# Performance work log

Measured on AMD Instinct MI355X. Metric: run time of the kernel, lower is better.

## Reference

```python
import jax, jax.numpy as jnp
import numpy as np

M = 1024      # num_inducing
B = 131072    # batch of query points (original module is per-query; we vmap/vectorize)
EPS_D = 1e-8
JITTER = 1e-4

Z_SCALE = np.array([0.15, 0.1, 0.05, 800.0, 20.0], dtype=np.float32)
Z_SHIFT = np.array([0.0, 0.0, 0.0, 600.0, 5.0], dtype=np.float32)


def setup_inputs() -> dict:
    key = jax.random.key(0)
    k1, k2 = jax.random.split(key)
    x_star = jax.random.normal(k1, (B, 5), dtype=jnp.float32)
    # learnable params, sized/initialized per the flax module
    log_lengthscale = jnp.log(jnp.array([0.2, 0.15, 0.1, 400.0, 15.0], dtype=jnp.float32))
    log_variance = jnp.asarray(jnp.log(0.08), dtype=jnp.float32)
    Z_raw = jax.random.uniform(k2, (M, 5), dtype=jnp.float32)  # uniform(scale=1.0) init
    return {"x_star": x_star, "log_lengthscale": log_lengthscale,
            "log_variance": log_variance, "Z_raw": Z_raw}


def _pairwise_sqdist(A, Bm):
    # ||a-b||^2 via gemm; A:(n,d), Bm:(m,d) -> (n,m)
    aa = jnp.sum(A * A, axis=-1)
    bb = jnp.sum(Bm * Bm, axis=-1)
    d2 = aa[:, None] + bb[None, :] - 2.0 * (A @ Bm.T)
    return jnp.maximum(d2, 0.0)


def _matern52(d2, prior_var):
    d = jnp.sqrt(d2 + EPS_D)
    s = jnp.sqrt(5.0) * d
    return prior_var * (1.0 + s + (5.0 / 3.0) * (d * d)) * jnp.exp(-s)


def reference(x_star, log_lengthscale, log_variance, Z_raw):
    ls = jnp.exp(log_lengthscale)                # (5,)
    prior_var = jnp.exp(log_variance)            # scalar
    Z = Z_raw * jnp.asarray(Z_SCALE) + jnp.asarray(Z_SHIFT)  # (M,5)
    inv_ls = 1.0 / (ls + 1e-8)
    Zs = Z * inv_ls                              # lengthscale-scaled inducing pts
    Xs = x_star * inv_ls                         # (B,5)

    K_ZZ = _matern52(_pairwise_sqdist(Zs, Zs), prior_var)            # (M,M)
    K_ZZ_inv = jnp.linalg.inv(K_ZZ + JITTER * jnp.eye(M, dtype=K_ZZ.dtype))

    k_xZ = _matern52(_pairwise_sqdist(Xs, Zs), prior_var)            # (B,M)
    red = jnp.sum(k_xZ * (k_xZ @ K_ZZ_inv), axis=-1)                 # (B,)
    variance = jnp.maximum(prior_var - red, 1e-6)
    return jnp.sqrt(variance)                                        # (B,) predictive std
```

## Files before the change

kernel.cpp:

```cpp
#include <hip/hip_runtime.h>
#include <math.h>

#define B_TOT 131072
#define M_N   1024
#define BS    128
#define NBK   8

typedef float    f32x4 __attribute__((ext_vector_type(4)));
typedef _Float16 f16x8 __attribute__((ext_vector_type(8)));

enum : size_t {
    OFF_KF  = 0,
    OFF_LF  = (size_t)4 << 20,
    OFF_WF  = (size_t)8 << 20,
    OFF_WPH = (size_t)12 << 20,
    OFF_WPL = (size_t)14 << 20,
    OFF_PF  = (size_t)16 << 20,
    OFF_ZT  = ((size_t)16 << 20) + 256,
};

__device__ __constant__ float c_zscale[5] = {0.15f, 0.1f, 0.05f, 800.0f, 20.0f};
__device__ __constant__ float c_zshift[5] = {0.0f, 0.0f, 0.0f, 600.0f, 5.0f};

__global__ __launch_bounds__(256) void k_build(const float* __restrict__ log_ls,
                                               const float* __restrict__ log_var,
                                               const float* __restrict__ Zraw,
                                               float* __restrict__ Kf,
                                               float* __restrict__ pf,
                                               float* __restrict__ Zst) {
    __shared__ float ps[6];
    __shared__ float zsi[5];
    int tid = threadIdx.x;
    if (tid < 5) ps[tid] = 1.0f / (__expf(log_ls[tid]) + 1e-8f);
    if (tid == 5) ps[5] = __expf(log_var[0]);
    __syncthreads();
    int i = blockIdx.x >> 2;
    int j = (blockIdx.x & 3) * 256 + tid;
    if (tid < 5) zsi[tid] = (Zraw[i * 5 + tid] * c_zscale[tid] + c_zshift[tid]) * ps[tid];
    __syncthreads();
    float d2 = 0.0f;
#pragma unroll
    for (int d = 0; d < 5; ++d) {
        float zj = (Zraw[j * 5 + d] * c_zscale[d] + c_zshift[d]) * ps[d];
        float df = zsi[d] - zj;
        d2 += df * df;
    }
    float dd = d2 + 1e-8f;
    float dist = sqrtf(dd);
    float s = 2.23606798f * dist;
    float v = ps[5] * (1.0f + s + 1.66666667f * dd) * __expf(-s);
    if (i == j) v += 1e-4f;
    Kf[(size_t)i * M_N + j] = v;
    if (blockIdx.x < 4) {
        int m = blockIdx.x * 256 + tid;
#pragma unroll
        for (int d = 0; d < 5; ++d)
            Zst[d * M_N + m] = (Zraw[m * 5 + d] * c_zscale[d] + c_zshift[d]) * ps[d];
    }
    if (blockIdx.x == 4 && tid < 6) pf[tid] = ps[tid];
}

__global__ __launch_bounds__(512) void kw_diag(float* __restrict__ Kf,
                                               float* __restrict__ Wf, int kb) {
    if (blockIdx.x) return;
    __shared__ float As[128][129];
    __shared__ float sinv[128];
    int tid = threadIdx.x;
    int r0 = kb * BS;
    for (int idx = tid; idx < BS * BS; idx += 512) {
        int rr = idx >> 7, cc = idx & 127;
        As[rr][cc] = Kf[(size_t)(r0 + rr) * M_N + r0 + cc];
    }
    __syncthreads();

    int r = tid & 127, q = tid >> 7;
    for (int p = 0; p < 16; ++p) {
        int j0 = p * 8;
        for (int j = j0; j < j0 + 8; ++j) {
            if (tid == j) {
                float d = sqrtf(As[j][j]);
                As[j][j] = d;
                sinv[j] = 1.0f / d;
            }
            __syncthreads();
            float arj = 0.0f;
            if (q == 0 && r > j) {
                arj = As[r][j] * sinv[j];
                As[r][j] = arj;
            }
            __syncthreads();
            if (q == 0 && r > j) {
#pragma unroll
                for (int c = j + 1; c < j0 + 8; ++c)
                    As[r][c] -= arj * As[c][j];
            }
        }
        __syncthreads();
        if (p < 15) {
            float a[8];
#pragma unroll
            for (int t = 0; t < 8; ++t) a[t] = As[r][j0 + t];
            for (int c = j0 + 8 + q; c < 128; c += 4) {
                if (r >= c) {
                    float s = As[r][c];
#pragma unroll
                    for (int t = 0; t < 8; ++t) s -= a[t] * As[c][j0 + t];
                    As[r][c] = s;
                }
            }
        }
        __syncthreads();
    }

    if (tid < 128) {
        int c = tid;
        for (int rb = 0; rb < 16; ++rb) {
            int r0b = rb * 8;
            if (c >= r0b + 8) continue;
            float s[8];
#pragma unroll
            for (int i = 0; i < 8; ++i) s[i] = 0.0f;
            for (int t = 0; t < r0b; ++t) {
                if (t >= c) {
                    float xt = (t == c) ? sinv[c] : As[c][t];
#pragma unroll
                    for (int i = 0; i < 8; ++i) s[i] += As[r0b + i][t] * xt;
                }
            }
            float xloc[8];
#pragma unroll
            for (int i = 0; i < 8; ++i) {
                int rr = r0b + i;
                float v = 0.0f;
                if (rr >= c) {
                    v = ((rr == c) ? 1.0f : 0.0f) - s[i];
#pragma unroll
                    for (int t2 = 0; t2 < i; ++t2) {
                        int tt = r0b + t2;
                        if (tt >= c) v -= As[rr][tt] * xloc[t2];
                    }
                    v *= sinv[rr];
                    if (rr > c) As[c][rr] = v;
                }
                xloc[i] = v;
            }
        }
    }
    __syncthreads();
    for (int idx = tid; idx < BS * BS; idx += 512) {
        int rr = idx >> 7, cc = idx & 127;
        if (rr >= cc)
            Wf[(size_t)(r0 + rr) * M_N + r0 + cc] = (rr == cc) ? sinv[rr] : As[cc][rr];
    }
}

static __device__ void d_strip(const float* __restrict__ Kf, const float* __restrict__ Wf,
                               int cb, int row0, float (*S)[129],
                               float (*Ast)[17], float (*Wst)[128], int tid) {
    int c = tid & 127, q = tid >> 7;
    float acc[32];
#pragma unroll
    for (int i = 0; i < 32; ++i) acc[i] = 0.0f;
    for (int tc = 0; tc < 8; ++tc) {
        int tb = tc * 16;
        __syncthreads();
        for (int idx = tid; idx < 64 * 16; idx += 256) {
            int rr = idx >> 4, tt = idx & 15;
            Ast[rr][tt] = Kf[(size_t)(row0 + rr) * M_N + cb + tb + tt];
        }
        for (int idx = tid; idx < 128 * 16; idx += 256) {
            int cc = idx >> 4, tt = idx & 15;
            Wst[tt][cc] = (tb + tt <= cc) ? Wf[(size_t)(cb + cc) * M_N + cb + tb + tt] : 0.0f;
        }
        __syncthreads();
#pragma unroll
        for (int t = 0; t < 16; ++t) {
            float w = Wst[t][c];
#pragma unroll
            for (int i = 0; i < 32; ++i) acc[i] += Ast[q * 32 + i][t] * w;
        }
    }
    __syncthreads();
#pragma unroll
    for (int i = 0; i < 32; ++i) S[q * 32 + i][c] = acc[i];
}

static __device__ void d_diag256(float (*As)[129], float* sinv,
                                 float* __restrict__ Wf, int r0, int tid) {
    int r = tid & 127, half = tid >> 7;
    for (int p = 0; p < 16; ++p) {
        int j0 = p * 8;
        for (int j = j0; j < j0 + 8; ++j) {
            if (tid == j) {
                float d = sqrtf(As[j][j]);
                As[j][j] = d;
                sinv[j] = 1.0f / d;
            }
            __syncthreads();
            float arj = 0.0f;
            if (half == 0 && r > j) {
                arj = As[r][j] * sinv[j];
                As[r][j] = arj;
            }
            __syncthreads();
            if (half == 0 && r > j) {
#pragma unroll
                for (int c = j + 1; c < j0 + 8; ++c)
                    As[r][c] -= arj * As[c][j];
            }
        }
        __syncthreads();
        if (p < 15) {
            float a[8];
#pragma unroll
            for (int t = 0; t < 8; ++t) a[t] = As[r][j0 + t];
            for (int c = j0 + 8 + half; c < 128; c += 2) {
                if (r >= c) {
                    float s = As[r][c];
#pragma unroll
                    for (int t = 0; t < 8; ++t) s -= a[t] * As[c][j0 + t];
                    As[r][c] = s;
                }
            }
        }
        __syncthreads();
    }
    if (tid < 128) {
        int c = tid;
        for (int rb = 0; rb < 16; ++rb) {
            int r0b = rb * 8;
            if (c >= r0b + 8) continue;
            float s[8];
#pragma unroll
            for (int i = 0; i < 8; ++i) s[i] = 0.0f;
            for (int t = 0; t < r0b; ++t) {
                if (t >= c) {
                    float xt = (t == c) ? sinv[c] : As[c][t];
#pragma unroll
                    for (int i = 0; i < 8; ++i) s[i] += As[r0b + i][t] * xt;
                }
            }
            float xloc[8];
#pragma unroll
            for (int i = 0; i < 8; ++i) {
                int rr = r0b + i;
                float v = 0.0f;
                if (rr >= c) {
                    v = ((rr == c) ? 1.0f : 0.0f) - s[i];
#pragma unroll
                    for (int t2 = 0; t2 < i; ++t2) {
                        int tt = r0b + t2;
                        if (tt >= c) v -= As[rr][tt] * xloc[t2];
                    }
                    v *= sinv[rr];
                    if (rr > c) As[c][rr] = v;
                }
                xloc[i] = v;
            }
        }
    }
    __syncthreads();
    for (int idx = tid; idx < BS * BS; idx += 256) {
        int rr = idx >> 7, cc = idx & 127;
        if (rr >= cc)
            Wf[(size_t)(r0 + rr) * M_N + r0 + cc] = (rr == cc) ? sinv[rr] : As[cc][rr];
    }
}

__global__ __launch_bounds__(256) void kw_step(float* __restrict__ Kf,
                                               float* __restrict__ Wf,
                                               float* __restrict__ Lf, int kb) {
    __shared__ float SA[64][129];
    __shared__ float SB[64][129];
    __shared__ float Ast[64][17];
    __shared__ float Wst[16][128];
    __shared__ float As[128][129];
    __shared__ float sinv[128];
    int tid = threadIdx.x;
    int base = (kb + 1) * BS;
    int cb = kb * BS;
    int tx = tid & 15, ty = tid >> 4;
    int nt = (NBK - 1 - kb) * 2;
    int ntile = nt * (nt + 1) / 2;

    if (blockIdx.x == 0) {
        d_strip(Kf, Wf, cb, base, SA, Ast, Wst, tid);
        d_strip(Kf, Wf, cb, base + 64, SB, Ast, Wst, tid);
        __syncthreads();
#pragma unroll
        for (int qq = 0; qq < 3; ++qq) {
            int qy = (qq == 0) ? 0 : 1;
            int qx = (qq == 2) ? 1 : 0;
            float (*Sy)[129] = qy ? SB : SA;
            float (*Sx)[129] = qx ? SB : SA;
            float acc[4][4];
#pragma unroll
            for (int i = 0; i < 4; ++i)
#pragma unroll
                for (int j = 0; j < 4; ++j) acc[i][j] = 0.0f;
            for (int t = 0; t < 128; ++t) {
                float a[4], b[4];
#pragma unroll
                for (int i = 0; i < 4; ++i) a[i] = Sy[ty * 4 + i][t];
#pragma unroll
                for (int j = 0; j < 4; ++j) b[j] = Sx[tx * 4 + j][t];
#pragma unroll
                for (int i = 0; i < 4; ++i)
#pragma unroll
                    for (int j = 0; j < 4; ++j) acc[i][j] = fmaf(a[i], b[j], acc[i][j]);
            }
#pragma unroll
            for (int i = 0; i < 4; ++i)
#pragma unroll
                for (int j = 0; j < 4; ++j)
                    As[qy * 64 + ty * 4 + i][qx * 64 + tx * 4 + j] =
                        Kf[(size_t)(base + qy * 64 + ty * 4 + i) * M_N +
                           base + qx * 64 + tx * 4 + j] - acc[i][j];
        }
        for (int idx = tid; idx < 64 * 128; idx += 256) {
            int rr = idx >> 7, cc = idx & 127;
            Lf[(size_t)(base + rr) * M_N + cb + cc]      = SA[rr][cc];
            Lf[(size_t)(base + 64 + rr) * M_N + cb + cc] = SB[rr][cc];
        }
        __syncthreads();
        d_diag256(As, sinv, Wf, base, tid);
    } else {
        int vp = blockIdx.x + 2;
        if (vp >= ntile) return;
        int by = 0;
        while ((by + 1) * (by + 2) / 2 <= vp) ++by;
        int bx = vp - by * (by + 1) / 2;
        int gr0 = base + by * 64, gc0 = base + bx * 64;
        d_strip(Kf, Wf, cb, gr0, SA, Ast, Wst, tid);
        if (bx != by) d_strip(Kf, Wf, cb, gc0, SB, Ast, Wst, tid);
        float (*PB)[129] = (bx == by) ? SA : SB;
        __syncthreads();
        float acc[4][4];
#pragma unroll
        for (int i = 0; i < 4; ++i)
#pragma unroll
            for (int j = 0; j < 4; ++j) acc[i][j] = 0.0f;
        for (int t = 0; t < 128; ++t) {
            float a[4], b[4];
#pragma unroll
            for (int i = 0; i < 4; ++i) a[i] = SA[ty * 4 + i][t];
#pragma unroll
            for (int j = 0; j < 4; ++j) b[j] = PB[tx * 4 + j][t];
#pragma unroll
            for (int i = 0; i < 4; ++i)
#pragma unroll
                for (int j = 0; j < 4; ++j) acc[i][j] = fmaf(a[i], b[j], acc[i][j]);
        }
#pragma unroll
        for (int i = 0; i < 4; ++i)
#pragma unroll
            for (int j = 0; j < 4; ++j)
                Kf[(size_t)(gr0 + ty * 4 + i) * M_N + gc0 + tx * 4 + j] -= acc[i][j];
        if (by == bx) {
            for (int idx = tid; idx < 64 * 128; idx += 256)
                Lf[(size_t)(gr0 + (idx >> 7)) * M_N + cb + (idx & 127)] =
                    SA[idx >> 7][idx & 127];
        }
    }
}

__global__ __launch_bounds__(512) void kw_trtri(const float* __restrict__ Lf,
                                                float* __restrict__ Wf) {
    __shared__ float Ls[128][33];
    __shared__ float Ws[32][33];
    __shared__ float Whist[6][128][33];
    __shared__ float Ps[128][33];
    int j  = blockIdx.y;
    int ct = blockIdx.x;
    int c0 = j * BS + ct * 32;
    int tid = threadIdx.x;
    int rq = tid >> 2, cq = tid & 3;

    for (int i = j + 1; i < 8; ++i) {
        float acc[8];
#pragma unroll
        for (int c = 0; c < 8; ++c) acc[c] = 0.0f;
        for (int t = j; t < i; ++t) {
            for (int ch = 0; ch < 4; ++ch) {
                int tb = t * BS + ch * 32;
                __syncthreads();
                for (int idx = tid; idx < 128 * 32; idx += 512) {
                    int rr = idx >> 5, tt = idx & 31;
                    Ls[rr][tt] = Lf[(size_t)(i * BS + rr) * M_N + tb + tt];
                }
                if (t == j) {
                    for (int idx = tid; idx < 32 * 32; idx += 512) {
                        int tt = idx >> 5, cc = idx & 31;
                        int gr = tb + tt, gc = c0 + cc;
                        Ws[tt][cc] = (gr >= gc) ? Wf[(size_t)gr * M_N + gc] : 0.0f;
                    }
                }
                __syncthreads();
                if (t == j) {
#pragma unroll
                    for (int tt = 0; tt < 32; ++tt) {
                        float l = Ls[rq][tt];
#pragma unroll
                        for (int c = 0; c < 8; ++c)
                            acc[c] = fmaf(l, Ws[tt][cq * 8 + c], acc[c]);
                    }
                } else {
                    const float (*Wh)[33] = Whist[t - j - 1];
#pragma unroll
                    for (int tt = 0; tt < 32; ++tt) {
                        float l = Ls[rq][tt];
#pragma unroll
                        for (int c = 0; c < 8; ++c)
                            acc[c] = fmaf(l, Wh[ch * 32 + tt][cq * 8 + c], acc[c]);
                    }
                }
            }
        }
        __syncthreads();
#pragma unroll
        for (int c = 0; c < 8; ++c) Ps[rq][cq * 8 + c] = acc[c];
        float a2[8];
#pragma unroll
        for (int c = 0; c < 8; ++c) a2[c] = 0.0f;
        for (int ch = 0; ch < 4; ++ch) {
            __syncthreads();
            for (int idx = tid; idx < 128 * 32; idx += 512) {
                int rr = idx >> 5, tt = idx & 31;
                Ls[rr][tt] = (rr >= ch * 32 + tt)
                           ? Wf[(size_t)(i * BS + rr) * M_N + i * BS + ch * 32 + tt] : 0.0f;
            }
            __syncthreads();
#pragma unroll
            for (int tt = 0; tt < 32; ++tt) {
                float l = Ls[rq][tt];
#pragma unroll
                for (int c = 0; c < 8; ++c)
                    a2[c] = fmaf(l, Ps[ch * 32 + tt][cq * 8 + c], a2[c]);
            }
        }
        __syncthreads();
#pragma unroll
        for (int c = 0; c < 8; ++c) {
            float v = -a2[c];
            Wf[(size_t)(i * BS + rq) * M_N + c0 + cq * 8 + c] = v;
            if (i < 7) Whist[i - j - 1][rq][cq * 8 + c] = v;
        }
        __syncthreads();
    }
}

__global__ void kw_pack(const float* __restrict__ Wf, _Float16* __restrict__ Wph,
                        _Float16* __restrict__ Wpl) {
    int T = blockIdx.x * 256 + threadIdx.x;
    int lane = T & 63, fid = T >> 6;
    int jn = fid & 63, kik = fid >> 6;
    int ki = kik & 3, kc = kik >> 2;
    int j  = jn * 16 + (lane & 15);
    int kb = kc * 128 + ki * 32 + (lane >> 4) * 8;
    f16x8 h, lo;
#pragma unroll
    for (int e = 0; e < 8; ++e) {
        int k = kb + e;
        float v = (k <= j) ? Wf[(size_t)j * M_N + k] : 0.0f;
        _Float16 hh = (_Float16)v;
        h[e]  = hh;
        lo[e] = (_Float16)(v - (float)hh);
    }
    size_t off = (size_t)fid * 512 + lane * 8;
    *(f16x8*)(Wph + off) = h;
    *(f16x8*)(Wpl + off) = lo;
}

__global__ __launch_bounds__(512, 2) void k_mm(const float* __restrict__ x_star,
                                               const float* __restrict__ pf,
                                               const float* __restrict__ Zst,
                                               const _Float16* __restrict__ Wph,
                                               const _Float16* __restrict__ Wpl,
                                               float* __restrict__ out, int Bq) {
    __shared__ __align__(16) char kls[64 * 256];
    __shared__ float red_l[64];
    int tid  = threadIdx.x;
    int slab = blockIdx.x;
    int w = tid >> 6, lane = tid & 63;
    int lrow = lane & 15, kgrp = lane >> 4;

    int scc = tid & 15, srow0 = tid >> 4;
    int q0 = slab * 64 + srow0;
    int q1 = q0 + 32;
    int qa = (q0 < Bq) ? q0 : (Bq - 1);
    int qb = (q1 < Bq) ? q1 : (Bq - 1);
    float xa0 = x_star[(size_t)qa * 5 + 0] * pf[0];
    float xa1 = x_star[(size_t)qa * 5 + 1] * pf[1];
    float xa2 = x_star[(size_t)qa * 5 + 2] * pf[2];
    float xa3 = x_star[(size_t)qa * 5 + 3] * pf[3];
    float xa4 = x_star[(size_t)qa * 5 + 4] * pf[4];
    float xb0 = x_star[(size_t)qb * 5 + 0] * pf[0];
    float xb1 = x_star[(size_t)qb * 5 + 1] * pf[1];
    float xb2 = x_star[(size_t)qb * 5 + 2] * pf[2];
    float xb3 = x_star[(size_t)qb * 5 + 3] * pf[3];
    float xb4 = x_star[(size_t)qb * 5 + 4] * pf[4];
    float pv = pf[5];
    if (tid < 64) red_l[tid] = 0.0f;

    int swz = (scc * 16) ^ ((srow0 & 15) << 4);
    int soff0 = srow0 * 256 + swz;
    int soff1 = (srow0 + 32) * 256 + swz;

    for (int pp = 0; pp < 2; ++pp) {
        f32x4 acc[4][4];
#pragma unroll
        for (int mi = 0; mi < 4; ++mi)
#pragma unroll
            for (int nj = 0; nj < 4; ++nj) acc[mi][nj] = (f32x4)(0.0f);

        int jmax_w = (pp * 32 + 24 + ((w + 3) & 7)) * 16 + 15;
        int KC = pp ? 8 : 4;

        for (int kc = 0; kc < KC; ++kc) {
            f16x8 h0, h1;
#pragma unroll
            for (int bb = 0; bb < 2; ++bb) {
                int lb = kc * 128 + scc * 8 + bb * 4;
                float z0[4], z1[4], z2[4], z3[4], z4[4];
                *(float4*)z0 = *(const float4*)&Zst[lb];
                *(float4*)z1 = *(const float4*)&Zst[M_N + lb];
                *(float4*)z2 = *(const float4*)&Zst[2 * M_N + lb];
                *(float4*)z3 = *(const float4*)&Zst[3 * M_N + lb];
                *(float4*)z4 = *(const float4*)&Zst[4 * M_N + lb];
#pragma unroll
                for (int e = 0; e < 4; ++e) {
                    float dx0 = xa0 - z0[e], dx1 = xa1 - z1[e], dx2 = xa2 - z2[e],
                          dx3 = xa3 - z3[e], dx4 = xa4 - z4[e];
                    float d2 = dx0 * dx0 + dx1 * dx1 + dx2 * dx2 + dx3 * dx3 + dx4 * dx4;
                    float dd = d2 + 1e-8f;
                    float dist = sqrtf(dd);
                    float sv = 2.23606798f * dist;
                    h0[bb * 4 + e] = (_Float16)(pv * (1.0f + sv + 1.66666667f * dd) * __expf(-sv));
                    float ex0 = xb0 - z0[e], ex1 = xb1 - z1[e], ex2 = xb2 - z2[e],
                          ex3 = xb3 - z3[e], ex4 = xb4 - z4[e];
                    float e2 = ex0 * ex0 + ex1 * ex1 + ex2 * ex2 + ex3 * ex3 + ex4 * ex4;
                    float ee = e2 + 1e-8f;
                    float edist = sqrtf(ee);
                    float esv = 2.23606798f * edist;
                    h1[bb * 4 + e] = (_Float16)(pv * (1.0f + esv + 1.66666667f * ee) * __expf(-esv));
                }
            }
            __syncthreads();
            *(f16x8*)(&kls[soff0]) = h0;
            *(f16x8*)(&kls[soff1]) = h1;
            __syncthreads();

            for (int ki = 0; ki < 4; ++ki) {
                int kmin = kc * 128 + ki * 32;
                if (kmin > jmax_w) break;
                f16x8 A_[4];
#pragma unroll
                for (int mi = 0; mi < 4; ++mi) {
                    int row = mi * 16 + lrow;
                    int cb  = ki * 64 + kgrp * 16;
                    A_[mi] = *(const f16x8*)(&kls[row * 256 + (cb ^ ((row & 15) << 4))]);
                }
#pragma unroll
                for (int nj = 0; nj < 4; ++nj) {
                    int jng = pp * 32 + nj * 8 + ((w + nj) & 7);
                    if (kmin > jng * 16 + 15) continue;
                    size_t fo = ((size_t)((kc * 4 + ki) * 64 + jng)) * 512 + lane * 8;
                    f16x8 Bh = *(const f16x8*)(Wph + fo);
                    f16x8 Bl = *(const f16x8*)(Wpl + fo);
#pragma unroll
                    for (int mi = 0; mi < 4; ++mi) {
                        acc[mi][nj] = __builtin_amdgcn_mfma_f32_16x16x32_f16(A_[mi], Bh, acc[mi][nj], 0, 0, 0);
                        acc[mi][nj] = __builtin_amdgcn_mfma_f32_16x16x32_f16(A_[mi], Bl, acc[mi][nj], 0, 0, 0);
                    }
                }
            }
        }

#pragma unroll
        for (int mi = 0; mi < 4; ++mi) {
#pragma unroll
            for (int q = 0; q < 4; ++q) {
                float s = 0.0f;
#pragma unroll
                for (int nj = 0; nj < 4; ++nj) s = fmaf(acc[mi][nj][q], acc[mi][nj][q], s);
                s += __shfl_xor(s, 1);
                s += __shfl_xor(s, 2);
                s += __shfl_xor(s, 4);
                s += __shfl_xor(s, 8);
                if (lrow == 0) atomicAdd(&red_l[mi * 16 + kgrp * 4 + q], s);
            }
        }
        __syncthreads();
    }

    if (tid < 64) {
        int b = slab * 64 + tid;
        if (b < Bq) out[b] = sqrtf(fmaxf(pv - red_l[tid], 1e-6f));
    }
}

extern "C" void kernel_launch(void* const* d_in, const int* in_sizes, int n_in,
                              void* d_out, int out_size, void* d_ws, size_t ws_size,
                              hipStream_t stream) {
    const float* x_star  = (const float*)d_in[0];
    const float* log_ls  = (const float*)d_in[1];
    const float* log_var = (const float*)d_in[2];
    const float* Z_raw   = (const float*)d_in[3];
    float* out = (float*)d_out;
    int Bq = in_sizes[0] / 5;

    char* ws = (char*)d_ws;
    float*     Kf  = (float*)(ws + OFF_KF);
    float*     Lf  = (float*)(ws + OFF_LF);
    float*     Wf  = (float*)(ws + OFF_WF);
    _Float16*  Wph = (_Float16*)(ws + OFF_WPH);
    _Float16*  Wpl = (_Float16*)(ws + OFF_WPL);
    float*     pf  = (float*)(ws + OFF_PF);
    float*     Zst = (float*)(ws + OFF_ZT);

    k_build<<<4096, 256, 0, stream>>>(log_ls, log_var, Z_raw, Kf, pf, Zst);
    kw_diag<<<64, 512, 0, stream>>>(Kf, Wf, 0);
    for (int kb = 0; kb < NBK - 1; ++kb) {
        int nt = (NBK - 1 - kb) * 2;
        int grid = nt * (nt + 1) / 2 - 2;
        if (grid < 64) grid = 64;
        kw_step<<<grid, 256, 0, stream>>>(Kf, Wf, Lf, kb);
    }
    kw_trtri<<<dim3(4, 7), 512, 0, stream>>>(Lf, Wf);
    kw_pack<<<512, 256, 0, stream>>>(Wf, Wph, Wpl);

    int slabs = (Bq + 63) / 64;
    k_mm<<<slabs, 512, 0, stream>>>(x_star, pf, Zst, Wph, Wpl, out, Bq);
}
```

Baseline: 3.510 ms.

## Compute full k_xZ row slab into LDS once, then sweep four column groups

The Matern kernel tile for all 1024 inducing points of a 64-query slab is now built once into a 128 KB LDS buffer. Previously each of two column passes rebuilt its K-chunks, so the first 512 columns' kernel values were computed twice. The matmul then loops over four column groups of two n-tiles each, cutting accumulators from 16 to 8 vectors, and drops the per-chunk double barriers. The cost is LDS use: 128 KB per block limits occupancy to one block per CU, which is why the launch-bounds minimum of 2 was removed. The exp/sqrt compute also no longer overlaps with MFMA work.

```diff
diff --git a/kernel.cpp b/kernel.cpp
--- a/kernel.cpp
+++ b/kernel.cpp
@@ -471,13 +471,13 @@
     *(f16x8*)(Wpl + off) = lo;
 }
 
-__global__ __launch_bounds__(512, 2) void k_mm(const float* __restrict__ x_star,
-                                               const float* __restrict__ pf,
-                                               const float* __restrict__ Zst,
-                                               const _Float16* __restrict__ Wph,
-                                               const _Float16* __restrict__ Wpl,
-                                               float* __restrict__ out, int Bq) {
-    __shared__ __align__(16) char kls[64 * 256];
+__global__ __launch_bounds__(512) void k_mm(const float* __restrict__ x_star,
+                                            const float* __restrict__ pf,
+                                            const float* __restrict__ Zst,
+                                            const _Float16* __restrict__ Wph,
+                                            const _Float16* __restrict__ Wpl,
+                                            float* __restrict__ out, int Bq) {
+    __shared__ __align__(16) char kls[64 * 2048];
     __shared__ float red_l[64];
     int tid  = threadIdx.x;
     int slab = blockIdx.x;
@@ -502,76 +502,73 @@
     float pv = pf[5];
     if (tid < 64) red_l[tid] = 0.0f;
 
-    int swz = (scc * 16) ^ ((srow0 & 15) << 4);
-    int soff0 = srow0 * 256 + swz;
-    int soff1 = (srow0 + 32) * 256 + swz;
-
-    for (int pp = 0; pp < 2; ++pp) {
-        f32x4 acc[4][4];
+    int swz = (srow0 & 15) << 4;
+    for (int kc = 0; kc < 8; ++kc) {
+        f16x8 h0, h1;
+#pragma unroll
+        for (int bb = 0; bb < 2; ++bb) {
+            int lb = kc * 128 + scc * 8 + bb * 4;
+            float z0[4], z1[4], z2[4], z3[4], z4[4];
+            *(float4*)z0 = *(const float4*)&Zst[lb];
+            *(float4*)z1 = *(const float4*)&Zst[M_N + lb];
+            *(float4*)z2 = *(const float4*)&Zst[2 * M_N + lb];
+            *(float4*)z3 = *(const float4*)&Zst[3 * M_N + lb];
+            *(float4*)z4 = *(const float4*)&Zst[4 * M_N + lb];
+#pragma unroll
+            for (int e = 0; e < 4; ++e) {
+                float dx0 = xa0 - z0[e], dx1 = xa1 - z1[e], dx2 = xa2 - z2[e],
+                      dx3 = xa3 - z3[e], dx4 = xa4 - z4[e];
+                float d2 = dx0 * dx0 + dx1 * dx1 + dx2 * dx2 + dx3 * dx3 + dx4 * dx4;
+                float dd = d2 + 1e-8f;
+                float dist = sqrtf(dd);
+                float sv = 2.23606798f * dist;
+                h0[bb * 4 + e] = (_Float16)(pv * (1.0f + sv + 1.66666667f * dd) * __expf(-sv));
+                float ex0 = xb0 - z0[e], ex1 = xb1 - z1[e], ex2 = xb2 - z2[e],
+                      ex3 = xb3 - z3[e], ex4 = xb4 - z4[e];
+                float e2 = ex0 * ex0 + ex1 * ex1 + ex2 * ex2 + ex3 * ex3 + ex4 * ex4;
+                float ee = e2 + 1e-8f;
+                float edist = sqrtf(ee);
+                float esv = 2.23606798f * edist;
+                h1[bb * 4 + e] = (_Float16)(pv * (1.0f + esv + 1.66666667f * ee) * __expf(-esv));
+            }
+        }
+        int cb = kc * 256 + scc * 16;
+        *(f16x8*)(&kls[srow0 * 2048 + (cb ^ swz)]) = h0;
+        *(f16x8*)(&kls[(srow0 + 32) * 2048 + (cb ^ swz)]) = h1;
+    }
+    __syncthreads();
+
+    for (int jg = 0; jg < 4; ++jg) {
+        f32x4 acc[4][2];
 #pragma unroll
         for (int mi = 0; mi < 4; ++mi)
 #pragma unroll
-            for (int nj = 0; nj < 4; ++nj) acc[mi][nj] = (f32x4)(0.0f);
-
-        int jmax_w = (pp * 32 + 24 + ((w + 3) & 7)) * 16 + 15;
-        int KC = pp ? 8 : 4;
-
-        for (int kc = 0; kc < KC; ++kc) {
-            f16x8 h0, h1;
-#pragma unroll
-            for (int bb = 0; bb < 2; ++bb) {
-                int lb = kc * 128 + scc * 8 + bb * 4;
-                float z0[4], z1[4], z2[4], z3[4], z4[4];
-                *(float4*)z0 = *(const float4*)&Zst[lb];
-                *(float4*)z1 = *(const float4*)&Zst[M_N + lb];
-                *(float4*)z2 = *(const float4*)&Zst[2 * M_N + lb];
-                *(float4*)z3 = *(const float4*)&Zst[3 * M_N + lb];
-                *(float4*)z4 = *(const float4*)&Zst[4 * M_N + lb];
-#pragma unroll
-                for (int e = 0; e < 4; ++e) {
-                    float dx0 = xa0 - z0[e], dx1 = xa1 - z1[e], dx2 = xa2 - z2[e],
-                          dx3 = xa3 - z3[e], dx4 = xa4 - z4[e];
-                    float d2 = dx0 * dx0 + dx1 * dx1 + dx2 * dx2 + dx3 * dx3 + dx4 * dx4;
-                    float dd = d2 + 1e-8f;
-                    float dist = sqrtf(dd);
-                    float sv = 2.23606798f * dist;
-                    h0[bb * 4 + e] = (_Float16)(pv * (1.0f + sv + 1.66666667f * dd) * __expf(-sv));
-                    float ex0 = xb0 - z0[e], ex1 = xb1 - z1[e], ex2 = xb2 - z2[e],
-                          ex3 = xb3 - z3[e], ex4 = xb4 - z4[e];
-                    float e2 = ex0 * ex0 + ex1 * ex1 + ex2 * ex2 + ex3 * ex3 + ex4 * ex4;
-                    float ee = e2 + 1e-8f;
-                    float edist = sqrtf(ee);
-                    float esv = 2.23606798f * edist;
-                    h1[bb * 4 + e] = (_Float16)(pv * (1.0f + esv + 1.66666667f * ee) * __expf(-esv));
-                }
-            }
-            __syncthreads();
-            *(f16x8*)(&kls[soff0]) = h0;
-            *(f16x8*)(&kls[soff1]) = h1;
-            __syncthreads();
-
-            for (int ki = 0; ki < 4; ++ki) {
-                int kmin = kc * 128 + ki * 32;
-                if (kmin > jmax_w) break;
-                f16x8 A_[4];
+            for (int nj = 0; nj < 2; ++nj) acc[mi][nj] = (f32x4)(0.0f);
+
+        int jng_hi = jg * 16 + 8 + ((w + 1) & 7);
+        int jmax_w = jng_hi * 16 + 15;
+
+        for (int kt = 0; kt < 32; ++kt) {
+            int kmin = kt * 32;
+            if (kmin > jmax_w) break;
+            f16x8 A_[4];
+#pragma unroll
+            for (int mi = 0; mi < 4; ++mi) {
+                int row = mi * 16 + lrow;
+                int cb  = kt * 64 + kgrp * 16;
+                A_[mi] = *(const f16x8*)(&kls[row * 2048 + (cb ^ ((row & 15) << 4))]);
+            }
+#pragma unroll
+            for (int nj = 0; nj < 2; ++nj) {
+                int jng = jg * 16 + nj * 8 + ((w + nj) & 7);
+                if (kmin > jng * 16 + 15) continue;
+                size_t fo = ((size_t)(kt * 64 + jng)) * 512 + lane * 8;
+                f16x8 Bh = *(const f16x8*)(Wph + fo);
+                f16x8 Bl = *(const f16x8*)(Wpl + fo);
 #pragma unroll
                 for (int mi = 0; mi < 4; ++mi) {
-                    int row = mi * 16 + lrow;
-                    int cb  = ki * 64 + kgrp * 16;
-                    A_[mi] = *(const f16x8*)(&kls[row * 256 + (cb ^ ((row & 15) << 4))]);
-                }
-#pragma unroll
-                for (int nj = 0; nj < 4; ++nj) {
-                    int jng = pp * 32 + nj * 8 + ((w + nj) & 7);
-                    if (kmin > jng * 16 + 15) continue;
-                    size_t fo = ((size_t)((kc * 4 + ki) * 64 + jng)) * 512 + lane * 8;
-                    f16x8 Bh = *(const f16x8*)(Wph + fo);
-                    f16x8 Bl = *(const f16x8*)(Wpl + fo);
-#pragma unroll
-                    for (int mi = 0; mi < 4; ++mi) {
-                        acc[mi][nj] = __builtin_amdgcn_mfma_f32_16x16x32_f16(A_[mi], Bh, acc[mi][nj], 0, 0, 0);
-                        acc[mi][nj] = __builtin_amdgcn_mfma_f32_16x16x32_f16(A_[mi], Bl, acc[mi][nj], 0, 0, 0);
-                    }
+                    acc[mi][nj] = __builtin_amdgcn_mfma_f32_16x16x32_f16(A_[mi], Bh, acc[mi][nj], 0, 0, 0);
+                    acc[mi][nj] = __builtin_amdgcn_mfma_f32_16x16x32_f16(A_[mi], Bl, acc[mi][nj], 0, 0, 0);
                 }
             }
         }
@@ -582,7 +579,7 @@
             for (int q = 0; q < 4; ++q) {
                 float s = 0.0f;
 #pragma unroll
-                for (int nj = 0; nj < 4; ++nj) s = fmaf(acc[mi][nj][q], acc[mi][nj][q], s);
+                for (int nj = 0; nj < 2; ++nj) s = fmaf(acc[mi][nj][q], acc[mi][nj][q], s);
                 s += __shfl_xor(s, 1);
                 s += __shfl_xor(s, 2);
                 s += __shfl_xor(s, 4);
@@ -590,9 +587,8 @@
                 if (lrow == 0) atomicAdd(&red_l[mi * 16 + kgrp * 4 + q], s);
             }
         }
-        __syncthreads();
-    }
-
+    }
+    __syncthreads();
     if (tid < 64) {
         int b = slab * 64 + tid;
         if (b < Bq) out[b] = sqrtf(fmaxf(pv - red_l[tid], 1e-6f));
```

New measurement: 3.477 ms. No clear change (-0.9%).
